# Optimization experiments

Measured on AMD Instinct MI355X. Metric: run time of the kernel, lower is better.

Reference implementation:

```python
import jax, jax.numpy as jnp
import numpy as np

EPS = 1e-12  # torch F.normalize default eps


def setup_inputs() -> dict:
    key = jax.random.key(0)
    k1, k2, k3, k4 = jax.random.split(key, 4)
    dim, heads, b, h, w = 192, 6, 2, 48, 48
    scale = 1.0 / np.sqrt(dim)
    return {
        "inp": jax.random.normal(k1, (b, dim, h, w), dtype=jnp.float32),
        "wq": jax.random.normal(k2, (dim, dim), dtype=jnp.float32) * scale,
        "wk": jax.random.normal(k3, (dim, dim), dtype=jnp.float32) * scale,
        "wv": jax.random.normal(k4, (dim, dim), dtype=jnp.float32) * scale,
        "temperature": jnp.ones((heads, 1, 1), dtype=jnp.float32),
    }


def _l2norm_lastdim(x):
    # torch F.normalize(x, dim=-1): x / max(||x||_2, eps)
    n = jnp.sqrt(jnp.sum(x * x, axis=-1, keepdims=True))
    return x / jnp.maximum(n, EPS)


def reference(inp, wq, wk, wv, temperature):
    b, c, h, w = inp.shape
    heads = temperature.shape[0]
    ch = c // heads
    n = h * w
    x = inp.reshape(b, c, n)  # 1x1 conv == channel matmul
    q = jnp.einsum("oc,bcn->bon", wq, x).reshape(b, heads, ch, n)
    k = jnp.einsum("oc,bcn->bon", wk, x).reshape(b, heads, ch, n)
    v = jnp.einsum("oc,bcn->bon", wv, x).reshape(b, heads, ch, n)
    q = _l2norm_lastdim(q)
    k = _l2norm_lastdim(k)
    # k^T @ q over channel dim -> [b, heads, n, n]; temperature [heads,1,1] broadcasts
    attn = jnp.einsum("bhcn,bhcm->bhnm", k, q) * temperature
    attn = jax.nn.softmax(attn, axis=-1)
    return attn, v
```

## Files before the change

### kernel.cpp

```cpp
#include <hip/hip_runtime.h>
#include <hip/hip_bf16.h>
#include <cstdint>

#define NSP   2304
#define NT    144
#define ATTN_ELEMS 63700992

typedef __attribute__((ext_vector_type(8))) __bf16 bf16x8;
typedef __attribute__((ext_vector_type(4))) float  float4v;

__device__ __forceinline__ unsigned short f2bf(float f) {
  union { float f; unsigned int u; } v; v.f = f;
  unsigned int u = v.u;
  unsigned int r = u + 0x7FFFu + ((u >> 16) & 1u);
  return (unsigned short)(r >> 16);
}

__global__ __launch_bounds__(256) void prep_pack(
    const float* __restrict__ wq, const float* __restrict__ wk,
    const float* __restrict__ wv, const float* __restrict__ x,
    unsigned short* __restrict__ Wp, unsigned short* __restrict__ Xp)
{
  int t = blockIdx.x * 256 + threadIdx.x;
  int lane = t & 63;
  int g = t >> 6;
  int quad = lane >> 4, col = lane & 15;
  union { int4 v; unsigned short u[8]; } o;
  if (g < 216) {
    int mt = g / 6, kc = g % 6;
    int oo = mt * 16 + col;
    int c0 = kc * 32 + quad * 8;
    const float* w = (oo < 192) ? (wq + (size_t)oo * 192)
                   : (oo < 384) ? (wk + (size_t)(oo - 192) * 192)
                                : (wv + (size_t)(oo - 384) * 192);
#pragma unroll
    for (int jj = 0; jj < 8; ++jj) o.u[jj] = f2bf(w[c0 + jj]);
    ((int4*)Wp)[(size_t)g * 64 + lane] = o.v;
  } else {
    int gx = g - 216;
    int kc = gx % 6;
    int bnt = gx / 6;
    int b = bnt / 144;
    int n = (bnt % 144) * 16 + col;
    int c0 = kc * 32 + quad * 8;
    const float* xp = x + ((size_t)b * 192 + c0) * NSP + n;
#pragma unroll
    for (int jj = 0; jj < 8; ++jj) o.u[jj] = f2bf(xp[(size_t)jj * NSP]);
    ((int4*)Xp)[(size_t)gx * 64 + lane] = o.v;
  }
}

__global__ __launch_bounds__(256) void proj_mfma(
    const bf16x8* __restrict__ Wp, const bf16x8* __restrict__ Xp,
    float* __restrict__ qws, float* __restrict__ kws, float* __restrict__ vout)
{
  int lane = threadIdx.x & 63, w = threadIdx.x >> 6;
  int ng = blockIdx.x * 4 + w;
  int mt = blockIdx.y;
  int b  = blockIdx.z;
  int nt0 = ng * 4;
  float4v acc0 = {0.f,0.f,0.f,0.f};
  float4v acc1 = acc0, acc2 = acc0, acc3 = acc0;
#pragma unroll
  for (int kc = 0; kc < 6; ++kc) {
    bf16x8 a = Wp[(size_t)(mt * 6 + kc) * 64 + lane];
    const bf16x8* xb = Xp + (size_t)((b * 144 + nt0) * 6 + kc) * 64 + lane;
    acc0 = __builtin_amdgcn_mfma_f32_16x16x32_bf16(a, xb[0],    acc0, 0, 0, 0);
    acc1 = __builtin_amdgcn_mfma_f32_16x16x32_bf16(a, xb[384],  acc1, 0, 0, 0);
    acc2 = __builtin_amdgcn_mfma_f32_16x16x32_bf16(a, xb[768],  acc2, 0, 0, 0);
    acc3 = __builtin_amdgcn_mfma_f32_16x16x32_bf16(a, xb[1152], acc3, 0, 0, 0);
  }
  int quad = lane >> 4, col = lane & 15;
  int o0 = mt * 16 + quad * 4;
  float* dst;
  if (mt < 12)      dst = qws + ((size_t)b * 192 + o0) * NSP;
  else if (mt < 24) dst = kws + ((size_t)b * 192 + (o0 - 192)) * NSP;
  else              dst = vout + ((size_t)b * 192 + (o0 - 384)) * NSP;
  float4v acc[4] = {acc0, acc1, acc2, acc3};
#pragma unroll
  for (int tt = 0; tt < 4; ++tt)
#pragma unroll
    for (int r = 0; r < 4; ++r)
      dst[(size_t)r * NSP + (nt0 + tt) * 16 + col] = acc[tt][r];
}

__global__ __launch_bounds__(256) void rownorm(
    const float* __restrict__ qws, const float* __restrict__ kws,
    float* __restrict__ inv)
{
  int r = blockIdx.x;
  const float* src = (r < 384) ? (qws + (size_t)r * NSP)
                               : (kws + (size_t)(r - 384) * NSP);
  float s = 0.f;
#pragma unroll
  for (int i = 0; i < 9; ++i) { float v = src[threadIdx.x + 256 * i]; s += v * v; }
#pragma unroll
  for (int off = 32; off > 0; off >>= 1) s += __shfl_down(s, off);
  __shared__ float ls[4];
  if ((threadIdx.x & 63) == 0) ls[threadIdx.x >> 6] = s;
  __syncthreads();
  if (threadIdx.x == 0) {
    float tot = ls[0] + ls[1] + ls[2] + ls[3];
    inv[r] = 1.0f / fmaxf(sqrtf(tot), 1e-12f);
  }
}

__global__ __launch_bounds__(256) void packqk(
    const float* __restrict__ qws, const float* __restrict__ kws,
    const float* __restrict__ inv,
    unsigned short* __restrict__ Qp, unsigned short* __restrict__ Kp)
{
  int which = blockIdx.z;
  int bh = blockIdx.y;
  int nc = blockIdx.x;
  const float* src = which ? kws : qws;
  const float* ivp = inv + which * 384;
  int b = bh / 6, h = bh % 6;
  __shared__ float xs[32][65];
  int t = threadIdx.x;
  const float* base = src + ((size_t)b * 192 + h * 32) * NSP + nc * 64;
#pragma unroll
  for (int i = 0; i < 8; ++i) {
    int idx = t + 256 * i;
    int ch = idx >> 6, nl = idx & 63;
    xs[ch][nl] = base[(size_t)ch * NSP + nl] * ivp[b * 192 + h * 32 + ch];
  }
  __syncthreads();
  int jl = t >> 6, lane = t & 63, quad = lane >> 4, col = lane & 15;
  int jt = nc * 4 + jl;
  union { int4 v; unsigned short u[8]; } o;
#pragma unroll
  for (int jj = 0; jj < 8; ++jj) o.u[jj] = f2bf(xs[quad * 8 + jj][jl * 16 + col]);
  int4* dst = (int4*)(which ? Kp : Qp);
  dst[(size_t)(bh * 144 + jt) * 64 + lane] = o.v;
}

__global__ __launch_bounds__(256) void attn_kernel(
    const bf16x8* __restrict__ Qp, const bf16x8* __restrict__ Kp,
    const float* __restrict__ temp, float* __restrict__ out)
{
  int lane = threadIdx.x & 63, w = threadIdx.x >> 6;
  int itile = blockIdx.x;
  int bh = blockIdx.y;
  float T = temp[bh % 6];
  bf16x8 a = Kp[((size_t)bh * NT + itile) * 64 + lane];
  const bf16x8* qb = Qp + (size_t)bh * NT * 64 + lane;
  int jt0 = w * 36;
  float l0 = 0.f, l1 = 0.f, l2 = 0.f, l3 = 0.f;
  for (int jt = jt0; jt < jt0 + 36; ++jt) {
    bf16x8 bf = qb[(size_t)jt * 64];
    float4v acc = {0.f,0.f,0.f,0.f};
    acc = __builtin_amdgcn_mfma_f32_16x16x32_bf16(a, bf, acc, 0, 0, 0);
    l0 += __expf(acc[0] * T);
    l1 += __expf(acc[1] * T);
    l2 += __expf(acc[2] * T);
    l3 += __expf(acc[3] * T);
  }
#pragma unroll
  for (int off = 1; off < 16; off <<= 1) {
    l0 += __shfl_xor(l0, off);
    l1 += __shfl_xor(l1, off);
    l2 += __shfl_xor(l2, off);
    l3 += __shfl_xor(l3, off);
  }
  int quad = lane >> 4, col = lane & 15;
  __shared__ float ls[4][16];
  if ((lane & 15) == 0) {
    ls[w][quad * 4 + 0] = l0; ls[w][quad * 4 + 1] = l1;
    ls[w][quad * 4 + 2] = l2; ls[w][quad * 4 + 3] = l3;
  }
  __syncthreads();
  float i0 = 1.0f / (ls[0][quad*4+0] + ls[1][quad*4+0] + ls[2][quad*4+0] + ls[3][quad*4+0]);
  float i1 = 1.0f / (ls[0][quad*4+1] + ls[1][quad*4+1] + ls[2][quad*4+1] + ls[3][quad*4+1]);
  float i2 = 1.0f / (ls[0][quad*4+2] + ls[1][quad*4+2] + ls[2][quad*4+2] + ls[3][quad*4+2]);
  float i3 = 1.0f / (ls[0][quad*4+3] + ls[1][quad*4+3] + ls[2][quad*4+3] + ls[3][quad*4+3]);
  float* ob = out + (size_t)bh * NSP * NSP + (size_t)(itile * 16 + quad * 4) * NSP + col;
  for (int jt = jt0; jt < jt0 + 36; ++jt) {
    bf16x8 bf = qb[(size_t)jt * 64];
    float4v acc = {0.f,0.f,0.f,0.f};
    acc = __builtin_amdgcn_mfma_f32_16x16x32_bf16(a, bf, acc, 0, 0, 0);
    ob[(size_t)0 * NSP + jt * 16] = __expf(acc[0] * T) * i0;
    ob[(size_t)1 * NSP + jt * 16] = __expf(acc[1] * T) * i1;
    ob[(size_t)2 * NSP + jt * 16] = __expf(acc[2] * T) * i2;
    ob[(size_t)3 * NSP + jt * 16] = __expf(acc[3] * T) * i3;
  }
}

extern "C" void kernel_launch(void* const* d_in, const int* in_sizes, int n_in,
                              void* d_out, int out_size, void* d_ws, size_t ws_size,
                              hipStream_t stream) {
  const float* x    = (const float*)d_in[0];
  const float* wq   = (const float*)d_in[1];
  const float* wk   = (const float*)d_in[2];
  const float* wv   = (const float*)d_in[3];
  const float* temp = (const float*)d_in[4];

  float* attn_out = (float*)d_out;
  float* vout     = attn_out + (size_t)ATTN_ELEMS;

  float* qws = (float*)d_ws;
  float* kws = qws + 884736;
  float* inv = kws + 884736;
  unsigned short* Wp = (unsigned short*)(inv + 768);
  unsigned short* Xp = Wp + 110592;
  unsigned short* Qp = Xp + 884736;
  unsigned short* Kp = Qp + 884736;

  hipLaunchKernelGGL(prep_pack, dim3(486), dim3(256), 0, stream,
                     wq, wk, wv, x, Wp, Xp);
  hipLaunchKernelGGL(proj_mfma, dim3(9, 36, 2), dim3(256), 0, stream,
                     (const bf16x8*)Wp, (const bf16x8*)Xp, qws, kws, vout);
  hipLaunchKernelGGL(rownorm, dim3(768), dim3(256), 0, stream, qws, kws, inv);
  hipLaunchKernelGGL(packqk, dim3(36, 12, 2), dim3(256), 0, stream,
                     qws, kws, inv, Qp, Kp);
  hipLaunchKernelGGL(attn_kernel, dim3(144, 12), dim3(256), 0, stream,
                     (const bf16x8*)Qp, (const bf16x8*)Kp, temp, attn_out);
}
```

Before: 281.3 us.

## Cache exp values in registers as bf16 and write transposed float4 rows

The attention kernel now uses 8 waves per block, and each wave handles 18 column tiles. Exponentials are computed once and kept in registers packed as bf16 pairs, so the second MFMA-and-exp pass is gone. The MFMA operands are swapped so each lane holds 4 consecutive columns of one row, which allows 16-byte float4 stores instead of scalar strided stores. Storing exp values in bf16 before normalising lowers the precision of the softmax output, and the extra registers may reduce occupancy.

```diff
diff --git a/kernel.cpp b/kernel.cpp
--- a/kernel.cpp
+++ b/kernel.cpp
@@ -14,6 +14,10 @@
   unsigned int u = v.u;
   unsigned int r = u + 0x7FFFu + ((u >> 16) & 1u);
   return (unsigned short)(r >> 16);
+}
+
+__device__ __forceinline__ float bf2f(unsigned int bits16) {
+  union { unsigned int u; float f; } v; v.u = bits16 << 16; return v.f;
 }
 
 __global__ __launch_bounds__(256) void prep_pack(
@@ -135,7 +139,7 @@
   dst[(size_t)(bh * 144 + jt) * 64 + lane] = o.v;
 }
 
-__global__ __launch_bounds__(256) void attn_kernel(
+__global__ __launch_bounds__(512) void attn_kernel(
     const bf16x8* __restrict__ Qp, const bf16x8* __restrict__ Kp,
     const float* __restrict__ temp, float* __restrict__ out)
 {
@@ -143,46 +147,47 @@
   int itile = blockIdx.x;
   int bh = blockIdx.y;
   float T = temp[bh % 6];
-  bf16x8 a = Kp[((size_t)bh * NT + itile) * 64 + lane];
+  bf16x8 kf = Kp[((size_t)bh * NT + itile) * 64 + lane];
   const bf16x8* qb = Qp + (size_t)bh * NT * 64 + lane;
-  int jt0 = w * 36;
-  float l0 = 0.f, l1 = 0.f, l2 = 0.f, l3 = 0.f;
-  for (int jt = jt0; jt < jt0 + 36; ++jt) {
-    bf16x8 bf = qb[(size_t)jt * 64];
+  int jt0 = w * 18;
+
+  unsigned int ec[36];
+  float s = 0.f;
+#pragma unroll
+  for (int u = 0; u < 18; ++u) {
+    bf16x8 qf = qb[(size_t)(jt0 + u) * 64];
     float4v acc = {0.f,0.f,0.f,0.f};
-    acc = __builtin_amdgcn_mfma_f32_16x16x32_bf16(a, bf, acc, 0, 0, 0);
-    l0 += __expf(acc[0] * T);
-    l1 += __expf(acc[1] * T);
-    l2 += __expf(acc[2] * T);
-    l3 += __expf(acc[3] * T);
-  }
-#pragma unroll
-  for (int off = 1; off < 16; off <<= 1) {
-    l0 += __shfl_xor(l0, off);
-    l1 += __shfl_xor(l1, off);
-    l2 += __shfl_xor(l2, off);
-    l3 += __shfl_xor(l3, off);
-  }
-  int quad = lane >> 4, col = lane & 15;
-  __shared__ float ls[4][16];
-  if ((lane & 15) == 0) {
-    ls[w][quad * 4 + 0] = l0; ls[w][quad * 4 + 1] = l1;
-    ls[w][quad * 4 + 2] = l2; ls[w][quad * 4 + 3] = l3;
-  }
+    acc = __builtin_amdgcn_mfma_f32_16x16x32_bf16(qf, kf, acc, 0, 0, 0);
+    float e0 = __expf(acc[0] * T);
+    float e1 = __expf(acc[1] * T);
+    float e2 = __expf(acc[2] * T);
+    float e3 = __expf(acc[3] * T);
+    s += (e0 + e1) + (e2 + e3);
+    ec[2*u]   = (unsigned int)f2bf(e0) | ((unsigned int)f2bf(e1) << 16);
+    ec[2*u+1] = (unsigned int)f2bf(e2) | ((unsigned int)f2bf(e3) << 16);
+  }
+  s += __shfl_xor(s, 16);
+  s += __shfl_xor(s, 32);
+  __shared__ float ls[8][16];
+  if (lane < 16) ls[w][lane] = s;
   __syncthreads();
-  float i0 = 1.0f / (ls[0][quad*4+0] + ls[1][quad*4+0] + ls[2][quad*4+0] + ls[3][quad*4+0]);
-  float i1 = 1.0f / (ls[0][quad*4+1] + ls[1][quad*4+1] + ls[2][quad*4+1] + ls[3][quad*4+1]);
-  float i2 = 1.0f / (ls[0][quad*4+2] + ls[1][quad*4+2] + ls[2][quad*4+2] + ls[3][quad*4+2]);
-  float i3 = 1.0f / (ls[0][quad*4+3] + ls[1][quad*4+3] + ls[2][quad*4+3] + ls[3][quad*4+3]);
-  float* ob = out + (size_t)bh * NSP * NSP + (size_t)(itile * 16 + quad * 4) * NSP + col;
-  for (int jt = jt0; jt < jt0 + 36; ++jt) {
-    bf16x8 bf = qb[(size_t)jt * 64];
-    float4v acc = {0.f,0.f,0.f,0.f};
-    acc = __builtin_amdgcn_mfma_f32_16x16x32_bf16(a, bf, acc, 0, 0, 0);
-    ob[(size_t)0 * NSP + jt * 16] = __expf(acc[0] * T) * i0;
-    ob[(size_t)1 * NSP + jt * 16] = __expf(acc[1] * T) * i1;
-    ob[(size_t)2 * NSP + jt * 16] = __expf(acc[2] * T) * i2;
-    ob[(size_t)3 * NSP + jt * 16] = __expf(acc[3] * T) * i3;
+  int col = lane & 15, quad = lane >> 4;
+  float tot = 0.f;
+#pragma unroll
+  for (int ww = 0; ww < 8; ++ww) tot += ls[ww][col];
+  float inv = 1.0f / tot;
+
+  float* ob = out + (size_t)bh * NSP * NSP
+            + (size_t)(itile * 16 + col) * NSP + quad * 4;
+#pragma unroll
+  for (int u = 0; u < 18; ++u) {
+    unsigned int p0 = ec[2*u], p1 = ec[2*u+1];
+    float4v o4;
+    o4[0] = bf2f(p0 & 0xffffu) * inv;
+    o4[1] = bf2f(p0 >> 16)     * inv;
+    o4[2] = bf2f(p1 & 0xffffu) * inv;
+    o4[3] = bf2f(p1 >> 16)     * inv;
+    *(float4v*)(ob + (size_t)(jt0 + u) * 16) = o4;
   }
 }
 
@@ -213,6 +218,6 @@
   hipLaunchKernelGGL(rownorm, dim3(768), dim3(256), 0, stream, qws, kws, inv);
   hipLaunchKernelGGL(packqk, dim3(36, 12, 2), dim3(256), 0, stream,
                      qws, kws, inv, Qp, Kp);
-  hipLaunchKernelGGL(attn_kernel, dim3(144, 12), dim3(256), 0, stream,
+  hipLaunchKernelGGL(attn_kernel, dim3(144, 12), dim3(512), 0, stream,
                      (const bf16x8*)Qp, (const bf16x8*)Kp, temp, attn_out);
 }
```

Result: slower. 287.9 us (+2.4%).
